# Kernel tuning notes

Measured on AMD Instinct MI355X. Metric: run time of the kernel, lower is better.

Reference implementation:

```python
import jax, jax.numpy as jnp
import numpy as np

B, S, D, H = 4, 2048, 1024, 16
HD = D // H


def setup_inputs() -> dict:
    key = jax.random.key(0)
    ks = jax.random.split(key, 12)
    sc = 0.02
    inp = {
        "q": jax.random.normal(ks[0], (B, S, D), jnp.float32),
        "k": jax.random.normal(ks[1], (B, S, D), jnp.float32),
        "v": jax.random.normal(ks[2], (B, S, D), jnp.float32),
        "mask": jnp.tril(jnp.ones((S, S), jnp.int32))[None, None],  # causal [1,1,S,S]
        "Wq": jax.random.normal(ks[3], (D, D), jnp.float32) * sc,
        "bq": jnp.zeros((D,), jnp.float32),
        "Wk": jax.random.normal(ks[4], (D, D), jnp.float32) * sc,
        "bk": jnp.zeros((D,), jnp.float32),
        "Wv": jax.random.normal(ks[5], (D, D), jnp.float32) * sc,
        "bv": jnp.zeros((D,), jnp.float32),
        "Wo": jax.random.normal(ks[6], (D, D), jnp.float32) * sc,
        "bo": jnp.zeros((D,), jnp.float32),
    }
    return inp


def reference(q, k, v, mask, Wq, bq, Wk, bk, Wv, bv, Wo, bo):
    # Linear projections (torch Linear: x @ W.T + b)
    qh = (q @ Wq.T + bq).reshape(B, S, H, HD).transpose(0, 2, 1, 3)  # [B,H,S,hd]
    kh = (k @ Wk.T + bk).reshape(B, S, H, HD).transpose(0, 2, 1, 3)
    vh = (v @ Wv.T + bv).reshape(B, S, H, HD).transpose(0, 2, 1, 3)
    score = jnp.einsum("bhqd,bhkd->bhqk", qh, kh) / jnp.sqrt(jnp.float32(HD))
    score = jnp.where(mask == 0, jnp.float32(-10000.0), score)
    attn = jax.nn.softmax(score, axis=-1)
    out = jnp.einsum("bhqk,bhkd->bhqd", attn, vh)  # [B,H,S,hd]
    out = out.transpose(0, 2, 1, 3).reshape(B, S, D)
    return out @ Wo.T + bo
```

## Files before the change

### kernel.cpp

```cpp
#include <hip/hip_runtime.h>

#define S_LEN 2048
#define D_DIM 1024
#define NB    4
#define NH    16
#define HDIM  64
#define QSCL  0.18033688011112042f

typedef float  f32x4  __attribute__((ext_vector_type(4)));
typedef __bf16 bf16x4 __attribute__((ext_vector_type(4)));
typedef __bf16 bf16x8 __attribute__((ext_vector_type(8)));

static __device__ __forceinline__ f32x4 mfma16(bf16x8 a, bf16x8 b, f32x4 c) {
  return __builtin_amdgcn_mfma_f32_16x16x32_bf16(a, b, c, 0, 0, 0);
}
static __device__ __forceinline__ bf16x4 cvt4(f32x4 v) {
  return __builtin_convertvector(v, bf16x4);
}
static __device__ __forceinline__ bf16x8 cvt8(f32x4 lo, f32x4 hi) {
  bf16x4 a = cvt4(lo), b = cvt4(hi);
  bf16x8 r;
  r[0] = a[0]; r[1] = a[1]; r[2] = a[2]; r[3] = a[3];
  r[4] = b[0]; r[5] = b[1]; r[6] = b[2]; r[7] = b[3];
  return r;
}
static __device__ __forceinline__ void cp16(const void* g, void* l) {
  __builtin_amdgcn_global_load_lds(
      (const __attribute__((address_space(1))) unsigned int*)g,
      (__attribute__((address_space(3))) unsigned int*)l, 16, 0, 0);
}

__global__ __launch_bounds__(256) void conv_w(
    const float* __restrict__ Wq, const float* __restrict__ Wk,
    const float* __restrict__ Wv, const float* __restrict__ Wo,
    __bf16* __restrict__ out)
{
  const float* src;
  if (blockIdx.y == 0) src = Wq;
  else if (blockIdx.y == 1) src = Wk;
  else if (blockIdx.y == 2) src = Wv;
  else src = Wo;
  size_t i = ((size_t)blockIdx.x * 256 + threadIdx.x) * 4;
  f32x4 v = *(const f32x4*)(src + i);
  *(bf16x4*)(out + (size_t)blockIdx.y * (D_DIM * D_DIM) + i) = cvt4(v);
}

static __device__ __forceinline__ void proj_epilogue(
    f32x4 (&acc)[4][4], int z, int mbase, int nbase, int wm, int wn,
    int l15, int quad, const float* bias,
    __bf16* qh, __bf16* kh, __bf16* vt)
{
  const float scl = (z == 0) ? QSCL : 1.0f;
#pragma unroll
  for (int mt = 0; mt < 4; ++mt)
#pragma unroll
    for (int nt = 0; nt < 4; ++nt) {
      int n = nbase + wn + nt * 16 + l15;
      int h = n >> 6, hd = n & 63;
      float bb = bias[n];
      f32x4 vv = acc[mt][nt];
#pragma unroll
      for (int r = 0; r < 4; ++r) vv[r] = (vv[r] + bb) * scl;
      bf16x4 pv = cvt4(vv);
      int m0 = mbase + wm + mt * 16 + quad * 4;
      int b = m0 >> 11, s0 = m0 & 2047;
      if (z == 2) {
        *(bf16x4*)(vt + ((size_t)((b * NH + h) * HDIM + hd)) * S_LEN + s0) = pv;
      } else {
        __bf16* out = (z == 0) ? qh : kh;
#pragma unroll
        for (int r = 0; r < 4; ++r)
          out[((size_t)(b * NH + h) * S_LEN + s0 + r) * HDIM + hd] = pv[r];
      }
    }
}

__global__ __launch_bounds__(256, 3) void proj_f32(
    const float* __restrict__ qin, const float* __restrict__ kin, const float* __restrict__ vin,
    const __bf16* __restrict__ Wbf,
    const float* __restrict__ bq, const float* __restrict__ bk, const float* __restrict__ bv,
    __bf16* __restrict__ qh, __bf16* __restrict__ kh, __bf16* __restrict__ vt)
{
  const float* A; const float* bias;
  if (blockIdx.z == 0)      { A = qin; bias = bq; }
  else if (blockIdx.z == 1) { A = kin; bias = bk; }
  else                      { A = vin; bias = bv; }
  const __bf16* W = Wbf + (size_t)blockIdx.z * (D_DIM * D_DIM);

  __shared__ float  As[128 * 64];
  __shared__ __bf16 Bs[128 * 64];

  const int tid  = threadIdx.x;
  const int wave = tid >> 6;
  const int lane = tid & 63;
  const int l15  = lane & 15;
  const int quad = lane >> 4;
  const int mbase = blockIdx.x * 128;
  const int nbase = blockIdx.y * 128;
  const int wm = (wave & 1) * 64;
  const int wn = (wave >> 1) * 64;
  const int arow = lane >> 4;
  const int brow = lane >> 3;

  f32x4 acc[4][4] = {};

  for (int kt = 0; kt < D_DIM; kt += 64) {
#pragma unroll
    for (int c = 0; c < 8; ++c) {
      int rr = c * 4 + arow;
      int r  = wave * 32 + rr;
      int col = ((lane & 15) ^ (rr & 15)) * 4;
      cp16(A + (size_t)(mbase + r) * D_DIM + kt + col, As + r * 64);
    }
#pragma unroll
    for (int c = 0; c < 4; ++c) {
      int r  = wave * 32 + c * 8 + brow;
      int col = ((lane & 7) ^ (brow & 7)) * 8;
      cp16(W + (size_t)(nbase + r) * D_DIM + kt + col, Bs + r * 64);
    }
    __syncthreads();

#pragma unroll
    for (int k0 = 0; k0 < 2; ++k0) {
      bf16x8 af[4], bfr[4];
#pragma unroll
      for (int i = 0; i < 4; ++i) {
        const float* ap = As + (wm + i * 16 + l15) * 64;
        int c0 = k0 * 8 + quad * 2;
        f32x4 lo = *(const f32x4*)(ap + ((c0 ^ l15) * 4));
        f32x4 hi = *(const f32x4*)(ap + (((c0 + 1) ^ l15) * 4));
        af[i] = cvt8(lo, hi);
        bfr[i] = *(const bf16x8*)(Bs + (wn + i * 16 + l15) * 64 +
                                  (((k0 * 4 + quad) ^ (l15 & 7)) * 8));
      }
#pragma unroll
      for (int mt = 0; mt < 4; ++mt)
#pragma unroll
        for (int nt = 0; nt < 4; ++nt)
          acc[mt][nt] = mfma16(af[mt], bfr[nt], acc[mt][nt]);
    }
    __syncthreads();
  }

  proj_epilogue(acc, blockIdx.z, mbase, nbase, wm, wn, l15, quad, bias, qh, kh, vt);
}

__global__ __launch_bounds__(256, 4) void attn_kernel(
    const __bf16* __restrict__ qh, const __bf16* __restrict__ kh,
    const __bf16* __restrict__ vt, __bf16* __restrict__ ao)
{
  __shared__ __bf16 Kb[2][64 * 64];
  __shared__ __bf16 Vb[2][64 * 64];

  const int lin = blockIdx.x + (blockIdx.y << 4);
  const int xcd = lin & 7;
  const int idx = lin >> 3;
  const int u   = idx & 15;
  const int x   = (u & 1) ? (15 - (u >> 1)) : (u >> 1);
  const int bh  = xcd * 8 + (idx >> 4);

  const int qc0 = x, qc1 = 31 - x;
  const int last = qc1;

  const __bf16* qp = qh + (size_t)bh * S_LEN * HDIM;
  const __bf16* kp = kh + (size_t)bh * S_LEN * HDIM;
  const __bf16* vp = vt + (size_t)bh * HDIM * S_LEN;

  const int tid  = threadIdx.x;
  const int wave = tid >> 6;
  const int lane = tid & 63;
  const int l15  = lane & 15;
  const int quad = lane >> 4;
  const int w16  = wave * 16;
  const int srow = lane >> 3;
  const int swz  = l15 & 7;
  const int vswz = ((l15 >> 3) << 2) | (l15 & 3);
  const int kr0  = ((l15 >> 2) << 3) | (l15 & 3);
  const int b = bh >> 4, h = bh & 15;

  bf16x8 fq[2][2];
#pragma unroll
  for (int j = 0; j < 2; ++j) {
    const int qb = (j ? qc1 : qc0) * 64;
    const __bf16* qrow = qp + (size_t)(qb + w16 + l15) * HDIM;
    fq[j][0] = *(const bf16x8*)(qrow + quad * 8);
    fq[j][1] = *(const bf16x8*)(qrow + 32 + quad * 8);
  }

  f32x4 accO[2][4] = {};
  float lp[2] = {0.f, 0.f};

#pragma unroll
  for (int c = 0; c < 2; ++c) {
    int rb = w16 + c * 8;
    int sc2 = (((lane & 7) ^ (((c & 1) << 2) | (srow & 3)))) * 8;
    cp16(kp + (size_t)(rb + srow) * HDIM + sc2, &Kb[0][rb * 64]);
    cp16(vp + (size_t)(rb + srow) * S_LEN + sc2, &Vb[0][rb * 64]);
  }

  int cur = 0;
  for (int kt = 0; kt <= last; ++kt) {
    __syncthreads();

    if (kt < last) {
#pragma unroll
      for (int c = 0; c < 2; ++c) {
        int rb = w16 + c * 8;
        int sc2 = (((lane & 7) ^ (((c & 1) << 2) | (srow & 3)))) * 8;
        cp16(kp + (size_t)((kt + 1) * 64 + rb + srow) * HDIM + sc2,
             &Kb[cur ^ 1][rb * 64]);
        cp16(vp + (size_t)(rb + srow) * S_LEN + (kt + 1) * 64 + sc2,
             &Vb[cur ^ 1][rb * 64]);
      }
    }

    const __bf16* Kc = &Kb[cur][0];
    const __bf16* Vc = &Vb[cur][0];
    const bool act0 = (kt <= qc0);

    f32x4 sc[2][4] = {};
    __builtin_amdgcn_s_setprio(1);
#pragma unroll
    for (int k0 = 0; k0 < 2; ++k0)
#pragma unroll
      for (int nt = 0; nt < 4; ++nt) {
        const int krow = kr0 + ((nt & 1) << 2) + ((nt >> 1) << 5);
        bf16x8 bk = *(const bf16x8*)(Kc + krow * 64 +
                                     (((k0 * 4 + quad) ^ swz) * 8));
        if (act0) sc[0][nt] = mfma16(bk, fq[0][k0], sc[0][nt]);
        sc[1][nt] = mfma16(bk, fq[1][k0], sc[1][nt]);
      }
    __builtin_amdgcn_s_setprio(0);

    bf16x8 pa[2][2];
#pragma unroll
    for (int j = 0; j < 2; ++j) {
      if (j == 0 && !act0) continue;
      const int qcj = j ? qc1 : qc0;
      f32x4 pf[4];
#pragma unroll
      for (int nt = 0; nt < 4; ++nt) {
#pragma unroll
        for (int r = 0; r < 4; ++r) pf[nt][r] = __builtin_amdgcn_exp2f(sc[j][nt][r]);
        if (kt == qcj) {
#pragma unroll
          for (int r = 0; r < 4; ++r) {
            int key = ((nt >> 1) << 5) + (quad << 3) + ((nt & 1) << 2) + r;
            if (key > w16 + l15) pf[nt][r] = 0.f;
          }
        }
      }
      f32x4 lv = (pf[0] + pf[1]) + (pf[2] + pf[3]);
      lp[j] += (lv[0] + lv[1]) + (lv[2] + lv[3]);
      pa[j][0] = cvt8(pf[0], pf[1]);
      pa[j][1] = cvt8(pf[2], pf[3]);
    }

    __builtin_amdgcn_s_setprio(1);
#pragma unroll
    for (int k0 = 0; k0 < 2; ++k0)
#pragma unroll
      for (int nt = 0; nt < 4; ++nt) {
        bf16x8 bv = *(const bf16x8*)(Vc + (nt * 16 + l15) * 64 +
                                     (((k0 * 4 + quad) ^ vswz) * 8));
        if (act0) accO[0][nt] = mfma16(pa[0][k0], bv, accO[0][nt]);
        accO[1][nt] = mfma16(pa[1][k0], bv, accO[1][nt]);
      }
    __builtin_amdgcn_s_setprio(0);

    cur ^= 1;
  }

#pragma unroll
  for (int j = 0; j < 2; ++j) {
    float lf = lp[j];
    lf += __shfl_xor(lf, 16);
    lf += __shfl_xor(lf, 32);
    const int qb = (j ? qc1 : qc0) * 64;
#pragma unroll
    for (int r = 0; r < 4; ++r) {
      float inv = 1.0f / __shfl(lf, quad * 4 + r);
#pragma unroll
      for (int nt = 0; nt < 4; ++nt) accO[j][nt][r] *= inv;
    }
#pragma unroll
    for (int nt = 0; nt < 4; ++nt) {
      bf16x4 ob = cvt4(accO[j][nt]);
#pragma unroll
      for (int r = 0; r < 4; ++r) {
        int sr = qb + w16 + quad * 4 + r;
        ao[((size_t)b * S_LEN + sr) * D_DIM + h * HDIM + nt * 16 + l15] = ob[r];
      }
    }
  }
}

__global__ __launch_bounds__(256, 4) void out_gemm(
    const __bf16* __restrict__ Ain, const __bf16* __restrict__ Wbf,
    const float* __restrict__ bo, float* __restrict__ Cout)
{
  __shared__ __bf16 As[128 * 64];
  __shared__ __bf16 Bs[128 * 64];

  const int tid  = threadIdx.x;
  const int wave = tid >> 6;
  const int lane = tid & 63;
  const int l15  = lane & 15;
  const int quad = lane >> 4;
  const int mbase = blockIdx.x * 128;
  const int nbase = blockIdx.y * 128;
  const int wm = (wave & 1) * 64;
  const int wn = (wave >> 1) * 64;
  const int brow = lane >> 3;
  const int scol = ((lane & 7) ^ (brow & 7)) * 8;
  const int swz  = l15 & 7;

  f32x4 acc[4][4] = {};

  for (int kt = 0; kt < D_DIM; kt += 64) {
#pragma unroll
    for (int c = 0; c < 4; ++c) {
      int r = wave * 32 + c * 8 + brow;
      cp16(Ain + (size_t)(mbase + r) * D_DIM + kt + scol, As + r * 64);
      cp16(Wbf + (size_t)(nbase + r) * D_DIM + kt + scol, Bs + r * 64);
    }
    __syncthreads();

#pragma unroll
    for (int k0 = 0; k0 < 2; ++k0) {
      bf16x8 af[4], bfr[4];
#pragma unroll
      for (int i = 0; i < 4; ++i) {
        int off = ((k0 * 4 + quad) ^ swz) * 8;
        af[i]  = *(const bf16x8*)(As + (wm + i * 16 + l15) * 64 + off);
        bfr[i] = *(const bf16x8*)(Bs + (wn + i * 16 + l15) * 64 + off);
      }
#pragma unroll
      for (int mt = 0; mt < 4; ++mt)
#pragma unroll
        for (int nt = 0; nt < 4; ++nt)
          acc[mt][nt] = mfma16(af[mt], bfr[nt], acc[mt][nt]);
    }
    __syncthreads();
  }

#pragma unroll
  for (int mt = 0; mt < 4; ++mt)
#pragma unroll
    for (int nt = 0; nt < 4; ++nt) {
      int n = nbase + wn + nt * 16 + l15;
      float bb = bo[n];
      int m0 = mbase + wm + mt * 16 + quad * 4;
#pragma unroll
      for (int r = 0; r < 4; ++r)
        Cout[(size_t)(m0 + r) * D_DIM + n] = acc[mt][nt][r] + bb;
    }
}

extern "C" void kernel_launch(void* const* d_in, const int* in_sizes, int n_in,
                              void* d_out, int out_size, void* d_ws, size_t ws_size,
                              hipStream_t stream) {
  const float* q  = (const float*)d_in[0];
  const float* k  = (const float*)d_in[1];
  const float* v  = (const float*)d_in[2];
  const float* Wq = (const float*)d_in[4];
  const float* bq = (const float*)d_in[5];
  const float* Wk = (const float*)d_in[6];
  const float* bk = (const float*)d_in[7];
  const float* Wv = (const float*)d_in[8];
  const float* bv = (const float*)d_in[9];
  const float* Wo = (const float*)d_in[10];
  const float* bo = (const float*)d_in[11];

  __bf16* ws = (__bf16*)d_ws;
  const size_t WSZ = (size_t)D_DIM * D_DIM;
  const size_t NE  = (size_t)NB * S_LEN * D_DIM;
  __bf16* wbf = ws;
  __bf16* qh  = ws + 4 * WSZ;
  __bf16* kh  = qh + NE;
  __bf16* vt  = kh + NE;
  __bf16* ao  = vt + NE;

  conv_w<<<dim3(1024, 4), 256, 0, stream>>>(Wq, Wk, Wv, Wo, wbf);
  proj_f32<<<dim3(64, 8, 3), 256, 0, stream>>>(q, k, v, wbf, bq, bk, bv, qh, kh, vt);
  attn_kernel<<<dim3(16, 64), 256, 0, stream>>>(qh, kh, vt, ao);
  out_gemm<<<dim3(64, 8), 256, 0, stream>>>(ao, wbf + 3 * WSZ, bo, (float*)d_out);
}
```

Measured before the change: 303.7 us.

## Register-prefetch fp32 activations and store bf16 tiles in LDS for projection GEMM

The projection kernel no longer copies fp32 activation tiles into shared memory. Each thread now loads the next K-tile into registers one iteration ahead, converts it to bf16 and writes it into a swizzled bf16 LDS tile. This halves LDS footprint and read traffic for A, removes the per-fragment conversion in the inner loop, and raises the occupancy target from 3 to 4 blocks. In exchange it uses more registers for the prefetch buffer and drops the direct global-to-LDS copy for A.

```diff
diff --git a/kernel.cpp b/kernel.cpp
--- a/kernel.cpp
+++ b/kernel.cpp
@@ -75,9 +75,9 @@
     }
 }
 
-__global__ __launch_bounds__(256, 3) void proj_f32(
-    const float* __restrict__ qin, const float* __restrict__ kin, const float* __restrict__ vin,
-    const __bf16* __restrict__ Wbf,
+__global__ __launch_bounds__(256, 4) void proj_fused(
+    const float* __restrict__ qin, const float* __restrict__ kin,
+    const float* __restrict__ vin, const __bf16* __restrict__ Wbf,
     const float* __restrict__ bq, const float* __restrict__ bk, const float* __restrict__ bv,
     __bf16* __restrict__ qh, __bf16* __restrict__ kh, __bf16* __restrict__ vt)
 {
@@ -87,7 +87,7 @@
   else                      { A = vin; bias = bv; }
   const __bf16* W = Wbf + (size_t)blockIdx.z * (D_DIM * D_DIM);
 
-  __shared__ float  As[128 * 64];
+  __shared__ __bf16 As[128 * 64];
   __shared__ __bf16 Bs[128 * 64];
 
   const int tid  = threadIdx.x;
@@ -99,39 +99,47 @@
   const int nbase = blockIdx.y * 128;
   const int wm = (wave & 1) * 64;
   const int wn = (wave >> 1) * 64;
-  const int arow = lane >> 4;
   const int brow = lane >> 3;
+  const int scol = ((lane & 7) ^ (brow & 7)) * 8;
+  const int swz  = l15 & 7;
 
   f32x4 acc[4][4] = {};
+  f32x4 rA[4][2];
+
+#pragma unroll
+  for (int c = 0; c < 4; ++c) {
+    const float* src = A + (size_t)(mbase + wave * 32 + c * 8 + brow) * D_DIM + scol;
+    rA[c][0] = *(const f32x4*)(src);
+    rA[c][1] = *(const f32x4*)(src + 4);
+  }
 
   for (int kt = 0; kt < D_DIM; kt += 64) {
 #pragma unroll
-    for (int c = 0; c < 8; ++c) {
-      int rr = c * 4 + arow;
-      int r  = wave * 32 + rr;
-      int col = ((lane & 15) ^ (rr & 15)) * 4;
-      cp16(A + (size_t)(mbase + r) * D_DIM + kt + col, As + r * 64);
-    }
-#pragma unroll
     for (int c = 0; c < 4; ++c) {
-      int r  = wave * 32 + c * 8 + brow;
-      int col = ((lane & 7) ^ (brow & 7)) * 8;
-      cp16(W + (size_t)(nbase + r) * D_DIM + kt + col, Bs + r * 64);
-    }
-    __syncthreads();
+      int r = wave * 32 + c * 8 + brow;
+      *(bf16x8*)(As + r * 64 + (lane & 7) * 8) = cvt8(rA[c][0], rA[c][1]);
+      cp16(W + (size_t)(nbase + r) * D_DIM + kt + scol, Bs + r * 64);
+    }
+    __syncthreads();
+
+    if (kt + 64 < D_DIM) {
+#pragma unroll
+      for (int c = 0; c < 4; ++c) {
+        const float* src = A + (size_t)(mbase + wave * 32 + c * 8 + brow) * D_DIM
+                           + (kt + 64) + scol;
+        rA[c][0] = *(const f32x4*)(src);
+        rA[c][1] = *(const f32x4*)(src + 4);
+      }
+    }
 
 #pragma unroll
     for (int k0 = 0; k0 < 2; ++k0) {
       bf16x8 af[4], bfr[4];
 #pragma unroll
       for (int i = 0; i < 4; ++i) {
-        const float* ap = As + (wm + i * 16 + l15) * 64;
-        int c0 = k0 * 8 + quad * 2;
-        f32x4 lo = *(const f32x4*)(ap + ((c0 ^ l15) * 4));
-        f32x4 hi = *(const f32x4*)(ap + (((c0 + 1) ^ l15) * 4));
-        af[i] = cvt8(lo, hi);
-        bfr[i] = *(const bf16x8*)(Bs + (wn + i * 16 + l15) * 64 +
-                                  (((k0 * 4 + quad) ^ (l15 & 7)) * 8));
+        int off = ((k0 * 4 + quad) ^ swz) * 8;
+        af[i]  = *(const bf16x8*)(As + (wm + i * 16 + l15) * 64 + off);
+        bfr[i] = *(const bf16x8*)(Bs + (wn + i * 16 + l15) * 64 + off);
       }
 #pragma unroll
       for (int mt = 0; mt < 4; ++mt)
@@ -382,7 +390,7 @@
   __bf16* ao  = vt + NE;
 
   conv_w<<<dim3(1024, 4), 256, 0, stream>>>(Wq, Wk, Wv, Wo, wbf);
-  proj_f32<<<dim3(64, 8, 3), 256, 0, stream>>>(q, k, v, wbf, bq, bk, bv, qh, kh, vt);
+  proj_fused<<<dim3(64, 8, 3), 256, 0, stream>>>(q, k, v, wbf, bq, bk, bv, qh, kh, vt);
   attn_kernel<<<dim3(16, 64), 256, 0, stream>>>(qh, kh, vt, ao);
   out_gemm<<<dim3(64, 8), 256, 0, stream>>>(ao, wbf + 3 * WSZ, bo, (float*)d_out);
 }
```

New measurement: 473.3 us. 1.56x slower.
